# Kernel tuning notes

Measured on AMD Instinct MI355X. Metric: run time of the kernel, lower is better.

Reference implementation:

```python
import jax, jax.numpy as jnp
import numpy as np

D_MODEL = 2048
N_HEADS = 16
D_HEAD = 128
INIT_RANGE = 0.02
EPSILON = -100000.0  # mask fill value from the original module


def setup_inputs() -> dict:
    key = jax.random.key(0)
    ks = jax.random.split(key, 6)
    x = jax.random.normal(ks[0], (2, 2048, D_MODEL), dtype=jnp.float32)
    W_Q = jax.random.normal(ks[1], (N_HEADS, D_MODEL, D_HEAD), dtype=jnp.float32) * INIT_RANGE
    W_K = jax.random.normal(ks[2], (N_HEADS, D_MODEL, D_HEAD), dtype=jnp.float32) * INIT_RANGE
    W_V = jax.random.normal(ks[3], (N_HEADS, D_MODEL, D_HEAD), dtype=jnp.float32) * INIT_RANGE
    W_O = jax.random.normal(ks[4], (N_HEADS, D_HEAD, D_MODEL), dtype=jnp.float32) * INIT_RANGE
    b_Q = jnp.zeros((N_HEADS, D_HEAD), dtype=jnp.float32)
    b_K = jnp.zeros((N_HEADS, D_HEAD), dtype=jnp.float32)
    b_V = jnp.zeros((N_HEADS, D_HEAD), dtype=jnp.float32)
    b_O = jnp.zeros((D_MODEL,), dtype=jnp.float32)
    return {"normalized_resid_pre": x, "W_Q": W_Q, "b_Q": b_Q, "W_K": W_K,
            "b_K": b_K, "W_V": W_V, "b_V": b_V, "W_O": W_O, "b_O": b_O}


def reference(normalized_resid_pre, W_Q, b_Q, W_K, b_K, W_V, b_V, W_O, b_O):
    x = normalized_resid_pre  # [b, s, d_model]
    # per-head projections: [b, s, h, d_head]
    q = jnp.einsum('bsd,hdk->bshk', x, W_Q) + b_Q
    k = jnp.einsum('bsd,hdk->bshk', x, W_K) + b_K
    v = jnp.einsum('bsd,hdk->bshk', x, W_V) + b_V
    # attention scores [b, h, q, k]
    scores = jnp.einsum('bqhk,bshk->bhqs', q, k) / jnp.sqrt(jnp.float32(D_HEAD))
    S = scores.shape[-1]
    causal = jnp.tril(jnp.ones((S, S), dtype=bool))  # True = keep
    scores = jnp.where(causal, scores, jnp.float32(EPSILON))
    pattern = jax.nn.softmax(scores, axis=-1)
    z = jnp.einsum('bhqs,bshk->bqhk', pattern, v)
    attn_out = jnp.einsum('bqhk,hkd->bqd', z, W_O) + b_O
    return attn_out
```

## Files before the change

kernel.cpp:

```cpp
#include <hip/hip_runtime.h>
#include <hip/hip_bf16.h>

typedef unsigned short bfu;
typedef short          bf16x8 __attribute__((ext_vector_type(8)));
typedef float          floatx4 __attribute__((ext_vector_type(4)));
typedef unsigned short bfu4 __attribute__((ext_vector_type(4)));
typedef unsigned int   u32x2 __attribute__((ext_vector_type(2)));

__device__ __forceinline__ bfu f2bf(float f) {
    __hip_bfloat16 h = __float2bfloat16(f);
    return __builtin_bit_cast(unsigned short, h);
}

__device__ __forceinline__ void glds16(const bfu* g, bfu* l) {
    __builtin_amdgcn_global_load_lds(
        (const __attribute__((address_space(1))) unsigned int*)g,
        (__attribute__((address_space(3))) unsigned int*)l, 16, 0, 0);
}

#define BATCH 2
#define SEQ   2048
#define DM    2048
#define NH    16
#define DKH   128
#define SCALE 0.08838834764831845f

__global__ __launch_bounds__(256)
void cvt_x(const float* __restrict__ x, bfu* __restrict__ xb, int n) {
    const int i = (blockIdx.x * 256 + threadIdx.x) * 4;
    if (i >= n) return;
    const float4 v = *(const float4*)(x + i);
    bfu4 p; p[0] = f2bf(v.x); p[1] = f2bf(v.y); p[2] = f2bf(v.z); p[3] = f2bf(v.w);
    *(bfu4*)(xb + i) = p;
}

__global__ __launch_bounds__(256)
void tcvt(const float* __restrict__ in, bfu* __restrict__ out, int R, int C, float s) {
    __shared__ float tile[32][33];
    const int bz = blockIdx.z;
    const float* src = in + (size_t)bz * R * C;
    bfu* dst = out + (size_t)bz * R * C;
    const int c0 = blockIdx.x * 32, r0 = blockIdx.y * 32;
    const int tx = threadIdx.x, ty = threadIdx.y;
    #pragma unroll
    for (int i = 0; i < 4; i++)
        tile[ty + i*8][tx] = src[(size_t)(r0 + ty + i*8) * C + c0 + tx];
    __syncthreads();
    #pragma unroll
    for (int i = 0; i < 4; i++)
        dst[(size_t)(c0 + ty + i*8) * R + r0 + tx] = f2bf(tile[tx][ty + i*8] * s);
}

__global__ __launch_bounds__(256)
void tcvt_qkv(const float* __restrict__ WQ, const float* __restrict__ WK,
              const float* __restrict__ WV,
              bfu* __restrict__ WtQ, bfu* __restrict__ WtK, bfu* __restrict__ WtV) {
    __shared__ float tile[32][33];
    const int p  = blockIdx.z >> 4;
    const int bz = blockIdx.z & 15;
    const float* src = (p == 0) ? WQ : (p == 1) ? WK : WV;
    bfu*         dst = (p == 0) ? WtQ : (p == 1) ? WtK : WtV;
    const float  s   = (p == 0) ? SCALE : 1.0f;
    src += (size_t)bz * DM * DKH;
    dst += (size_t)bz * DM * DKH;
    const int c0 = blockIdx.x * 32, r0 = blockIdx.y * 32;
    const int tx = threadIdx.x, ty = threadIdx.y;
    #pragma unroll
    for (int i = 0; i < 4; i++)
        tile[ty + i*8][tx] = src[(size_t)(r0 + ty + i*8) * DKH + c0 + tx];
    __syncthreads();
    #pragma unroll
    for (int i = 0; i < 4; i++)
        dst[(size_t)(c0 + ty + i*8) * DM + r0 + tx] = f2bf(tile[tx][ty + i*8] * s);
}

__global__ __launch_bounds__(256)
void proj_qkv(const bfu* __restrict__ xb,
              const bfu* __restrict__ WtQ, const bfu* __restrict__ WtK,
              const bfu* __restrict__ WtV,
              const float* __restrict__ bQ, const float* __restrict__ bK,
              const float* __restrict__ bV,
              bfu* __restrict__ Qall, bfu* __restrict__ Kall, bfu* __restrict__ Vt) {
    __shared__ bfu As[128 * 32];
    __shared__ bfu Bs[128 * 32];
    const int p = blockIdx.y >> 4;
    const bfu*   Wt   = (p == 0) ? WtQ : (p == 1) ? WtK : WtV;
    const float* bias = (p == 0) ? bQ  : (p == 1) ? bK  : bV;
    const float bscale = (p == 0) ? SCALE : 1.0f;

    const int tid  = threadIdx.x;
    const int lane = tid & 63;
    const int wave = tid >> 6;
    const int lrow = lane & 15;
    const int quad = lane >> 4;
    const int mw = (wave & 1) * 64;
    const int nw = (wave >> 1) * 64;
    const size_t m0 = (size_t)blockIdx.x * 128;
    const size_t n0 = (size_t)(blockIdx.y & 15) * 128;
    const int rowb = lane >> 2;
    const int colb = (lane & 3) * 8;

    floatx4 acc[4][4] = {};

    for (int k0 = 0; k0 < DM; k0 += 32) {
        __syncthreads();
        #pragma unroll
        for (int i = 0; i < 2; i++) {
            const int rg = wave * 2 + i;
            glds16(xb + (m0 + rg*16 + rowb) * DM + k0 + colb, &As[rg * 512]);
            glds16(Wt + (n0 + rg*16 + rowb) * DM + k0 + colb, &Bs[rg * 512]);
        }
        __syncthreads();
        bf16x8 af[4], bfr[4];
        #pragma unroll
        for (int t = 0; t < 4; t++) {
            af[t]  = *(const bf16x8*)&As[(mw + t*16 + lrow) * 32 + quad * 8];
            bfr[t] = *(const bf16x8*)&Bs[(nw + t*16 + lrow) * 32 + quad * 8];
        }
        #pragma unroll
        for (int mt = 0; mt < 4; mt++)
            #pragma unroll
            for (int nt = 0; nt < 4; nt++)
                acc[mt][nt] = __builtin_amdgcn_mfma_f32_16x16x32_bf16(
                                  af[mt], bfr[nt], acc[mt][nt], 0, 0, 0);
    }

    if (p < 2) {
        bfu* Out = (p == 0) ? Qall : Kall;
        #pragma unroll
        for (int mt = 0; mt < 4; mt++) {
            #pragma unroll
            for (int nt = 0; nt < 4; nt++) {
                const int nl = (int)n0 + nw + nt*16 + lrow;
                const float bv = bias[nl] * bscale;
                #pragma unroll
                for (int r = 0; r < 4; r++) {
                    const size_t gm = m0 + mw + mt*16 + quad*4 + r;
                    Out[gm * DM + nl] = f2bf(acc[mt][nt][r] + bv);
                }
            }
        }
    } else {
        #pragma unroll
        for (int mt = 0; mt < 4; mt++) {
            #pragma unroll
            for (int nt = 0; nt < 4; nt++) {
                const int nl = (int)n0 + nw + nt*16 + lrow;
                const float bv = bias[nl] * bscale;
                const size_t gm0 = m0 + mw + mt*16 + quad*4;
                const int b = (int)(gm0 >> 11), s = (int)(gm0 & 2047);
                bfu4 pk;
                #pragma unroll
                for (int r = 0; r < 4; r++) pk[r] = f2bf(acc[mt][nt][r] + bv);
                *(bfu4*)&Vt[((size_t)(b * NH + (nl >> 7)) * DKH + (nl & 127)) * SEQ + s] = pk;
            }
        }
    }
}

__global__ __launch_bounds__(256)
void flash_attn(const bfu* __restrict__ Q, const bfu* __restrict__ K,
                const bfu* __restrict__ Vt, bfu* __restrict__ Z) {
    __shared__ bfu Ks[4][64][32];
    __shared__ bfu Vs[2][128][32];
    __shared__ bfu Ps[4][16][72];

    const int tid  = threadIdx.x;
    const int lane = tid & 63;
    const int wave = tid >> 6;
    const int lrow = lane & 15;
    const int quad = lane >> 4;
    const int hb = blockIdx.x;
    const int h = hb & 15, b = hb >> 4;
    const int qt = 31 - blockIdx.y;
    const int q0w = qt * 64 + wave * 16;
    const int rowb = lane >> 2, colb = (lane & 3) * 8;

    const bfu* Qrow = Q + (size_t)(b * SEQ + q0w + lrow) * DM + h * DKH;
    bf16x8 qf[4];
    #pragma unroll
    for (int kc = 0; kc < 4; kc++)
        qf[kc] = *(const bf16x8*)(Qrow + kc*32 + quad*8);

    floatx4 z[8] = {};
    float l_loc = 0.f;
    const int qg = q0w + lrow;

    const bfu* Kb = K + (size_t)b * SEQ * DM + h * DKH;
    const bfu* Vb = Vt + (size_t)(b * NH + h) * DKH * SEQ;
    const int ntiles = qt + 1;

    for (int it = 0; it < ntiles; it++) {
        const int s0 = it * 64;
        __syncthreads();
        #pragma unroll
        for (int i = 0; i < 8; i++) {
            const int chunk = wave * 8 + i;
            if (chunk < 16) {
                const int kc = chunk >> 2, kg = chunk & 3;
                glds16(Kb + (size_t)(s0 + kg*16 + rowb) * DM + kc*32 + colb,
                       &Ks[kc][kg*16][0]);
            } else {
                const int c2 = chunk - 16;
                const int sh = c2 >> 3, dg = c2 & 7;
                glds16(Vb + (size_t)(dg*16 + rowb) * SEQ + s0 + sh*32 + colb,
                       &Vs[sh][dg*16][0]);
            }
        }
        __syncthreads();

        floatx4 sc[4];
        #pragma unroll
        for (int st = 0; st < 4; st++) {
            floatx4 a = {};
            #pragma unroll
            for (int kc = 0; kc < 4; kc++) {
                bf16x8 kf = *(const bf16x8*)&Ks[kc][st*16 + lrow][quad*8];
                a = __builtin_amdgcn_mfma_f32_16x16x32_bf16(kf, qf[kc], a, 0, 0, 0);
            }
            sc[st] = a;
        }

        #pragma unroll
        for (int st = 0; st < 4; st++) {
            const int sbase = s0 + st*16 + quad*4;
            const float p0 = (sbase + 0 <= qg) ? __expf(sc[st][0]) : 0.f;
            const float p1 = (sbase + 1 <= qg) ? __expf(sc[st][1]) : 0.f;
            const float p2 = (sbase + 2 <= qg) ? __expf(sc[st][2]) : 0.f;
            const float p3 = (sbase + 3 <= qg) ? __expf(sc[st][3]) : 0.f;
            l_loc += (p0 + p1) + (p2 + p3);
            u32x2 pk;
            pk[0] = (unsigned)f2bf(p0) | ((unsigned)f2bf(p1) << 16);
            pk[1] = (unsigned)f2bf(p2) | ((unsigned)f2bf(p3) << 16);
            *(u32x2*)&Ps[wave][lrow][st*16 + quad*4] = pk;
        }

        bf16x8 pf0 = *(const bf16x8*)&Ps[wave][lrow][quad*8];
        bf16x8 pf1 = *(const bf16x8*)&Ps[wave][lrow][32 + quad*8];
        #pragma unroll
        for (int dt = 0; dt < 8; dt++) {
            bf16x8 v0 = *(const bf16x8*)&Vs[0][dt*16 + lrow][quad*8];
            z[dt] = __builtin_amdgcn_mfma_f32_16x16x32_bf16(pf0, v0, z[dt], 0, 0, 0);
            bf16x8 v1 = *(const bf16x8*)&Vs[1][dt*16 + lrow][quad*8];
            z[dt] = __builtin_amdgcn_mfma_f32_16x16x32_bf16(pf1, v1, z[dt], 0, 0, 0);
        }
    }

    float L = l_loc;
    L += __shfl_xor(L, 16);
    L += __shfl_xor(L, 32);
    float inv[4];
    #pragma unroll
    for (int r = 0; r < 4; r++)
        inv[r] = 1.0f / __shfl(L, quad*4 + r, 64);
    #pragma unroll
    for (int dt = 0; dt < 8; dt++) {
        #pragma unroll
        for (int r = 0; r < 4; r++) {
            const int qq = q0w + quad*4 + r;
            const int dk = dt*16 + lrow;
            Z[(size_t)(b * SEQ + qq) * DM + h * DKH + dk] = f2bf(z[dt][r] * inv[r]);
        }
    }
}

__global__ __launch_bounds__(256)
void out_gemm(const bfu* __restrict__ Zb, const bfu* __restrict__ WtO,
              const float* __restrict__ bO, float* out) {
    __shared__ bfu As[128 * 32];
    __shared__ bfu Bs[128 * 32];
    const int tid  = threadIdx.x;
    const int lane = tid & 63;
    const int wave = tid >> 6;
    const int lrow = lane & 15;
    const int quad = lane >> 4;
    const int mw = (wave & 1) * 64;
    const int nw = (wave >> 1) * 64;
    const size_t m0 = (size_t)blockIdx.x * 128;
    const size_t n0 = (size_t)blockIdx.y * 128;
    const int rowb = lane >> 2, colb = (lane & 3) * 8;

    floatx4 acc[4][4] = {};

    for (int k0 = 0; k0 < DM; k0 += 32) {
        __syncthreads();
        #pragma unroll
        for (int i = 0; i < 2; i++) {
            const int rg = wave * 2 + i;
            glds16(Zb  + (m0 + rg*16 + rowb) * DM + k0 + colb, &As[rg * 512]);
            glds16(WtO + (n0 + rg*16 + rowb) * DM + k0 + colb, &Bs[rg * 512]);
        }
        __syncthreads();
        bf16x8 af[4], bfr[4];
        #pragma unroll
        for (int t = 0; t < 4; t++) {
            af[t]  = *(const bf16x8*)&As[(mw + t*16 + lrow) * 32 + quad * 8];
            bfr[t] = *(const bf16x8*)&Bs[(nw + t*16 + lrow) * 32 + quad * 8];
        }
        #pragma unroll
        for (int mt = 0; mt < 4; mt++)
            #pragma unroll
            for (int nt = 0; nt < 4; nt++)
                acc[mt][nt] = __builtin_amdgcn_mfma_f32_16x16x32_bf16(
                                  af[mt], bfr[nt], acc[mt][nt], 0, 0, 0);
    }

    #pragma unroll
    for (int mt = 0; mt < 4; mt++) {
        #pragma unroll
        for (int nt = 0; nt < 4; nt++) {
            const size_t gn = n0 + nw + nt*16 + lrow;
            const float bv = bO[gn];
            #pragma unroll
            for (int r = 0; r < 4; r++) {
                const size_t gm = m0 + mw + mt*16 + quad*4 + r;
                out[gm * DM + gn] = acc[mt][nt][r] + bv;
            }
        }
    }
}

extern "C" void kernel_launch(void* const* d_in, const int* in_sizes, int n_in,
                              void* d_out, int out_size, void* d_ws, size_t ws_size,
                              hipStream_t stream) {
    const float* x  = (const float*)d_in[0];
    const float* WQ = (const float*)d_in[1];
    const float* bQ = (const float*)d_in[2];
    const float* WK = (const float*)d_in[3];
    const float* bK = (const float*)d_in[4];
    const float* WV = (const float*)d_in[5];
    const float* bV = (const float*)d_in[6];
    const float* WO = (const float*)d_in[7];
    const float* bO = (const float*)d_in[8];
    float* out = (float*)d_out;
    bfu* ws  = (bfu*)d_ws;
    bfu* dob = (bfu*)d_out;

    bfu* Qall = ws;
    bfu* Kall = Qall + 8388608;
    bfu* Vt   = Kall + 8388608;
    bfu* Zb   = Vt   + 8388608;
    bfu* WtV  = Zb;
    bfu* xb   = dob;
    bfu* WtQ  = dob + 8388608;
    bfu* WtK  = dob + 12582912;

    const dim3 tb(32, 8, 1);

    cvt_x<<<8192, 256, 0, stream>>>(x, xb, BATCH * SEQ * DM);

    tcvt_qkv<<<dim3(4, 64, 48), tb, 0, stream>>>(WQ, WK, WV, WtQ, WtK, WtV);
    proj_qkv<<<dim3(32, 48), 256, 0, stream>>>(xb, WtQ, WtK, WtV,
                                               bQ, bK, bV, Qall, Kall, Vt);

    flash_attn<<<dim3(32, 32), 256, 0, stream>>>(Qall, Kall, Vt, Zb);

    tcvt<<<dim3(64, 64, 1), tb, 0, stream>>>(WO, Qall, DM, DM, 1.0f);
    out_gemm<<<dim3(32, 16), 256, 0, stream>>>(Zb, Qall, bO, out);
}
```

Measured before the change: 368.8 us.

## Rewrite QKV projection as 256x256 tiled, double-buffered 8-wave GEMM with swizzled LDS

```diff
diff --git a/kernel.cpp b/kernel.cpp
--- a/kernel.cpp
+++ b/kernel.cpp
@@ -74,85 +74,178 @@
         dst[(size_t)(c0 + ty + i*8) * DM + r0 + tx] = f2bf(tile[tx][ty + i*8] * s);
 }
 
-__global__ __launch_bounds__(256)
-void proj_qkv(const bfu* __restrict__ xb,
-              const bfu* __restrict__ WtQ, const bfu* __restrict__ WtK,
-              const bfu* __restrict__ WtV,
-              const float* __restrict__ bQ, const float* __restrict__ bK,
-              const float* __restrict__ bV,
-              bfu* __restrict__ Qall, bfu* __restrict__ Kall, bfu* __restrict__ Vt) {
-    __shared__ bfu As[128 * 32];
-    __shared__ bfu Bs[128 * 32];
-    const int p = blockIdx.y >> 4;
+__device__ __forceinline__ void stg_half(const bfu* gbase, bfu* slot,
+                                         int wave, int lane, int csw) {
+    #pragma unroll
+    for (int l = 0; l < 2; l++) {
+        const int j = l * 8 + wave;
+        glds16(gbase + (size_t)((j >> 1) * 16 + (lane >> 2)) * DM
+                     + (j & 1) * 32 + csw,
+               slot + j * 512);
+    }
+}
+
+__device__ __forceinline__ void ld_b8(bf16x8 (&bv)[4][2], const bfu* slot, int rdo) {
+    #pragma unroll
+    for (int n = 0; n < 4; n++)
+        #pragma unroll
+        for (int ks = 0; ks < 2; ks++)
+            bv[n][ks] = *(const bf16x8*)&slot[(n * 2 + ks) * 512 + rdo];
+}
+
+__device__ __forceinline__ void ld_a8(bf16x8 (&af)[4][2], const bfu* slot, int rdo) {
+    #pragma unroll
+    for (int m = 0; m < 4; m++)
+        #pragma unroll
+        for (int ks = 0; ks < 2; ks++)
+            af[m][ks] = *(const bf16x8*)&slot[(m * 2 + ks) * 512 + rdo];
+}
+
+template<int MH, int NHALF>
+__device__ __forceinline__ void mfma16(floatx4 (&acc)[8][4],
+                                       const bf16x8 (&af)[4][2],
+                                       const bf16x8 (&bv)[4][2]) {
+    __builtin_amdgcn_s_setprio(1);
+    #pragma unroll
+    for (int m = 0; m < 4; m++)
+        #pragma unroll
+        for (int n = 0; n < 2; n++)
+            #pragma unroll
+            for (int ks = 0; ks < 2; ks++)
+                acc[MH*4 + m][NHALF*2 + n] =
+                    __builtin_amdgcn_mfma_f32_16x16x32_bf16(
+                        af[m][ks], bv[NHALF*2 + n][ks],
+                        acc[MH*4 + m][NHALF*2 + n], 0, 0, 0);
+    __builtin_amdgcn_s_setprio(0);
+}
+
+#define BARW()                                                      \
+    __builtin_amdgcn_s_barrier();                                   \
+    asm volatile("s_waitcnt lgkmcnt(0)" ::: "memory");              \
+    __builtin_amdgcn_sched_barrier(0)
+
+__global__ __launch_bounds__(512, 2)
+void proj_qkv8(const bfu* __restrict__ xb,
+               const bfu* __restrict__ WtQ, const bfu* __restrict__ WtK,
+               const bfu* __restrict__ WtV,
+               const float* __restrict__ bQ, const float* __restrict__ bK,
+               const float* __restrict__ bV,
+               bfu* __restrict__ Qall, bfu* __restrict__ Kall, bfu* __restrict__ Vt) {
+    __shared__ __align__(16) bfu As[2][2][8192];
+    __shared__ __align__(16) bfu Bs[2][2][8192];
+
+    const int p = blockIdx.y >> 3;
     const bfu*   Wt   = (p == 0) ? WtQ : (p == 1) ? WtK : WtV;
     const float* bias = (p == 0) ? bQ  : (p == 1) ? bK  : bV;
-    const float bscale = (p == 0) ? SCALE : 1.0f;
+    const float  bscale = (p == 0) ? SCALE : 1.0f;
 
     const int tid  = threadIdx.x;
     const int lane = tid & 63;
     const int wave = tid >> 6;
     const int lrow = lane & 15;
     const int quad = lane >> 4;
-    const int mw = (wave & 1) * 64;
-    const int nw = (wave >> 1) * 64;
-    const size_t m0 = (size_t)blockIdx.x * 128;
-    const size_t n0 = (size_t)(blockIdx.y & 15) * 128;
-    const int rowb = lane >> 2;
-    const int colb = (lane & 3) * 8;
-
-    floatx4 acc[4][4] = {};
-
-    for (int k0 = 0; k0 < DM; k0 += 32) {
-        __syncthreads();
-        #pragma unroll
-        for (int i = 0; i < 2; i++) {
-            const int rg = wave * 2 + i;
-            glds16(xb + (m0 + rg*16 + rowb) * DM + k0 + colb, &As[rg * 512]);
-            glds16(Wt + (n0 + rg*16 + rowb) * DM + k0 + colb, &Bs[rg * 512]);
-        }
-        __syncthreads();
-        bf16x8 af[4], bfr[4];
-        #pragma unroll
-        for (int t = 0; t < 4; t++) {
-            af[t]  = *(const bf16x8*)&As[(mw + t*16 + lrow) * 32 + quad * 8];
-            bfr[t] = *(const bf16x8*)&Bs[(nw + t*16 + lrow) * 32 + quad * 8];
-        }
-        #pragma unroll
-        for (int mt = 0; mt < 4; mt++)
-            #pragma unroll
-            for (int nt = 0; nt < 4; nt++)
-                acc[mt][nt] = __builtin_amdgcn_mfma_f32_16x16x32_bf16(
-                                  af[mt], bfr[nt], acc[mt][nt], 0, 0, 0);
-    }
+    const int wr   = wave >> 2;
+    const int wc   = wave & 3;
+    const size_t m0 = (size_t)blockIdx.x * 256;
+    const int    n0 = (int)(blockIdx.y & 7) * 256;
+
+    const int csw = ((lane & 3) * 8) ^ ((lane & 32) ? 16 : 0);
+    const int rdo = lrow * 32 + ((quad * 8) ^ ((lrow & 8) ? 16 : 0));
+
+    const bfu* Ab = xb + m0 * DM;
+    const bfu* Bb = Wt + (size_t)n0 * DM;
+
+    floatx4 acc[8][4] = {};
+    bf16x8 af[4][2], bv[4][2];
+
+#define STAGE_A(tau, h)                                                     \
+    if ((tau) < 32) stg_half(Ab + (size_t)((h) * 128) * DM + (tau) * 64,    \
+                             &As[(tau) & 1][h][0], wave, lane, csw)
+#define STAGE_B(tau, h)                                                     \
+    if ((tau) < 32) stg_half(Bb + (size_t)((h) * 128) * DM + (tau) * 64,    \
+                             &Bs[(tau) & 1][h][0], wave, lane, csw)
+
+    STAGE_B(0, 0); STAGE_B(0, 1); STAGE_A(0, 0); STAGE_A(0, 1);
+    STAGE_B(1, 0); STAGE_B(1, 1); STAGE_A(1, 0);
+    asm volatile("s_waitcnt vmcnt(6)" ::: "memory");
+    __builtin_amdgcn_s_barrier();
+
+    #pragma unroll 1
+    for (int i = 0; i < 16; i++) {
+        const int t0 = 2 * i;
+        ld_b8(bv, &Bs[0][wc >> 1][(wc & 1) * 4096], rdo);
+        ld_a8(af, &As[0][wr][0], rdo);
+        STAGE_A(t0 + 1, 1);
+        BARW();
+        mfma16<0, 0>(acc, af, bv);
+        __builtin_amdgcn_s_barrier();
+        STAGE_B(t0 + 2, 0);
+        BARW();
+        mfma16<0, 1>(acc, af, bv);
+        __builtin_amdgcn_s_barrier();
+        ld_a8(af, &As[0][wr][4096], rdo);
+        STAGE_B(t0 + 2, 1);
+        BARW();
+        mfma16<1, 0>(acc, af, bv);
+        __builtin_amdgcn_s_barrier();
+        STAGE_A(t0 + 2, 0);
+        BARW();
+        mfma16<1, 1>(acc, af, bv);
+        if (i == 15) asm volatile("s_waitcnt vmcnt(0)" ::: "memory");
+        else         asm volatile("s_waitcnt vmcnt(6)" ::: "memory");
+        __builtin_amdgcn_s_barrier();
+        ld_b8(bv, &Bs[1][wc >> 1][(wc & 1) * 4096], rdo);
+        ld_a8(af, &As[1][wr][0], rdo);
+        STAGE_A(t0 + 2, 1);
+        BARW();
+        mfma16<0, 0>(acc, af, bv);
+        __builtin_amdgcn_s_barrier();
+        STAGE_B(t0 + 3, 0);
+        BARW();
+        mfma16<0, 1>(acc, af, bv);
+        __builtin_amdgcn_s_barrier();
+        ld_a8(af, &As[1][wr][4096], rdo);
+        STAGE_B(t0 + 3, 1);
+        BARW();
+        mfma16<1, 0>(acc, af, bv);
+        __builtin_amdgcn_s_barrier();
+        STAGE_A(t0 + 3, 0);
+        BARW();
+        mfma16<1, 1>(acc, af, bv);
+        if (i < 15) asm volatile("s_waitcnt vmcnt(6)" ::: "memory");
+        __builtin_amdgcn_s_barrier();
+    }
+#undef STAGE_A
+#undef STAGE_B
 
     if (p < 2) {
         bfu* Out = (p == 0) ? Qall : Kall;
         #pragma unroll
-        for (int mt = 0; mt < 4; mt++) {
-            #pragma unroll
-            for (int nt = 0; nt < 4; nt++) {
-                const int nl = (int)n0 + nw + nt*16 + lrow;
-                const float bv = bias[nl] * bscale;
+        for (int m = 0; m < 8; m++) {
+            #pragma unroll
+            for (int n = 0; n < 4; n++) {
+                const int gn = n0 + wc * 64 + n * 16 + lrow;
+                const float bvv = bias[gn] * bscale;
                 #pragma unroll
                 for (int r = 0; r < 4; r++) {
-                    const size_t gm = m0 + mw + mt*16 + quad*4 + r;
-                    Out[gm * DM + nl] = f2bf(acc[mt][nt][r] + bv);
+                    const size_t gm = m0 + wr * 128 + m * 16 + quad * 4 + r;
+                    Out[gm * DM + gn] = f2bf(acc[m][n][r] + bvv);
                 }
             }
         }
     } else {
         #pragma unroll
-        for (int mt = 0; mt < 4; mt++) {
-            #pragma unroll
-            for (int nt = 0; nt < 4; nt++) {
-                const int nl = (int)n0 + nw + nt*16 + lrow;
-                const float bv = bias[nl] * bscale;
-                const size_t gm0 = m0 + mw + mt*16 + quad*4;
+        for (int m = 0; m < 8; m++) {
+            #pragma unroll
+            for (int n = 0; n < 4; n++) {
+                const int gn = n0 + wc * 64 + n * 16 + lrow;
+                const float bvv = bias[gn];
+                const size_t gm0 = m0 + wr * 128 + m * 16 + quad * 4;
                 const int b = (int)(gm0 >> 11), s = (int)(gm0 & 2047);
                 bfu4 pk;
                 #pragma unroll
-                for (int r = 0; r < 4; r++) pk[r] = f2bf(acc[mt][nt][r] + bv);
-                *(bfu4*)&Vt[((size_t)(b * NH + (nl >> 7)) * DKH + (nl & 127)) * SEQ + s] = pk;
+                for (int r = 0; r < 4; r++) pk[r] = f2bf(acc[m][n][r] + bvv);
+                *(bfu4*)&Vt[((size_t)(b * NH + (gn >> 7)) * DKH + (gn & 127)) * SEQ + s] = pk;
             }
         }
     }
@@ -350,8 +443,8 @@
     cvt_x<<<8192, 256, 0, stream>>>(x, xb, BATCH * SEQ * DM);
 
     tcvt_qkv<<<dim3(4, 64, 48), tb, 0, stream>>>(WQ, WK, WV, WtQ, WtK, WtV);
-    proj_qkv<<<dim3(32, 48), 256, 0, stream>>>(xb, WtQ, WtK, WtV,
-                                               bQ, bK, bV, Qall, Kall, Vt);
+    proj_qkv8<<<dim3(16, 24), 512, 0, stream>>>(xb, WtQ, WtK, WtV,
+                                                bQ, bK, bV, Qall, Kall, Vt);
 
     flash_attn<<<dim3(32, 32), 256, 0, stream>>>(Qall, Kall, Vt, Zb);
 
```

New measurement: 376.9 us. 2.2% more time.
